# Kernel optimization log

Hardware: AMD Instinct MI355X
Metric: run time of the kernel (lower is better)

The kernel has to match this reference:

```python
import jax, jax.numpy as jnp
import numpy as np

B_, L_, D_ = 2, 1024, 2048
E_, N_, R_, K_ = 4096, 16, 128, 4
EPS = 1e-5


def setup_inputs() -> dict:
    key = jax.random.key(0)
    ks = jax.random.split(key, 12)
    s = lambda i, shape, scale=0.02: jax.random.normal(ks[i], shape, jnp.float32) * scale
    # dt bias init as in the module: inv_dt = dt + log(-expm1(-dt)), dt ~ logU[1e-3, 0.1]
    dt = jnp.exp(jax.random.uniform(ks[10], (E_,)) * (np.log(0.1) - np.log(0.001)) + np.log(0.001))
    inv_dt = dt + jnp.log(-jnp.expm1(-dt))
    return {
        'resid': jax.random.normal(ks[0], (B_, L_, D_), jnp.float32),
        'norm_w': jnp.ones((D_,), jnp.float32),
        'skip_w': s(1, (E_, D_)),
        'in_w': s(2, (E_, D_)),
        'conv_w': s(3, (E_, K_), 0.2),
        'conv_b': jnp.zeros((E_,), jnp.float32),
        'wd1': s(4, (R_, E_)),
        'wd2': s(5, (E_, R_), R_ ** -0.5),
        'wd2_b': inv_dt,
        'wB': s(6, (N_, E_)),
        'wC': s(7, (N_, E_)),
        'A_log': jnp.log(jnp.broadcast_to(jnp.arange(1, N_ + 1, dtype=jnp.float32), (E_, N_))),
        'W_D': jnp.ones((E_,), jnp.float32),
        'out_w': s(8, (D_, E_)),
    }


def _forward(resid, norm_w, skip_w, in_w, conv_w, conv_b, wd1, wd2, wd2_b,
             wB, wC, A_log, W_D, out_w):
    B, L, D = resid.shape
    E, K = conv_w.shape
    N = A_log.shape[1]
    # RMSNorm
    rn = resid * jax.lax.rsqrt(jnp.mean(resid * resid, -1, keepdims=True) + EPS) * norm_w
    skip = rn @ skip_w.T                       # [B,L,E] gate branch (z)
    x_in = rn @ in_w.T                         # [B,L,E]
    # depthwise causal conv1d (pad left K-1, truncate to L), then SiLU
    xp = jnp.pad(x_in, ((0, 0), (K - 1, 0), (0, 0)))
    conv = conv_b + sum(xp[:, k:k + L, :] * conv_w[:, k] for k in range(K))
    x = jax.nn.silu(conv)                      # [B,L,E] ssm input
    # low-rank delta, input-dependent B/C
    delta = jax.nn.softplus((x @ wd1.T) @ wd2.T + wd2_b)   # [B,L,E]
    A = -jnp.exp(A_log)                        # [E,N]
    Bm = x @ wB.T                              # [B,L,N]
    Cm = x @ wC.T                              # [B,L,N]

    def step(h, inp):
        d_l, b_l, c_l, x_l = inp               # [B,E],[B,N],[B,N],[B,E]
        h = jnp.exp(d_l[:, :, None] * A) * h + (d_l * x_l)[:, :, None] * b_l[:, None, :]
        y_l = jnp.einsum('ben,bn->be', h, c_l)
        return h, y_l

    h0 = jnp.zeros((B, E, N), resid.dtype)
    xs = (delta.transpose(1, 0, 2), Bm.transpose(1, 0, 2),
          Cm.transpose(1, 0, 2), x.transpose(1, 0, 2))
    _, ys = jax.lax.scan(step, h0, xs)         # ys: [L,B,E]
    y = ys.transpose(1, 0, 2) + x * W_D        # skip connection via D
    y = y * jax.nn.silu(skip)                  # gating
    return resid + y @ out_w.T                 # out_proj + residual


def reference(resid, norm_w, skip_w, in_w, conv_w, conv_b, wd1, wd2, wd2_b,
              wB, wC, A_log, W_D, out_w):
    return _forward(resid, norm_w, skip_w, in_w, conv_w, conv_b, wd1, wd2,
                    wd2_b, wB, wC, A_log, W_D, out_w)
```

## Files before the change

kernel.cpp:

```cpp
#include <hip/hip_runtime.h>
#include <stdint.h>

#define NB 2
#define NL 1024
#define ND 2048
#define NE 4096
#define NN 16
#define NR 128
#define NKC 4
#define NBL (NB*NL)
#define EPSV 1e-5f
#define SEG_T 256
#define SCAN_T 32

typedef __attribute__((ext_vector_type(4))) float f32x4;
typedef __attribute__((ext_vector_type(8))) short short8;
typedef __attribute__((ext_vector_type(8))) unsigned short ushort8;
typedef __attribute__((ext_vector_type(4))) unsigned short ushort4_t;
typedef __attribute__((ext_vector_type(2))) unsigned short ushort2_t;

__device__ __forceinline__ unsigned short f2bf(float f) {
  union { float f; unsigned u; } v; v.f = f;
  unsigned r = v.u + 0x7FFFu + ((v.u >> 16) & 1u);
  return (unsigned short)(r >> 16);
}

__device__ __forceinline__ float bf2f(unsigned short u) {
  union { unsigned u; float f; } v; v.u = (unsigned)u << 16; return v.f;
}

__device__ __forceinline__ void load_lds16(const void* g, void* l) {
  __builtin_amdgcn_global_load_lds((const __attribute__((address_space(1))) void*)g,
                                   (__attribute__((address_space(3))) void*)l,
                                   16, 0, 0);
}

__device__ __forceinline__ int swzmask(int row) {
  return ((row ^ (row >> 2)) & 3) * 8;
}

template<int CTRL>
__device__ __forceinline__ float dpp_mov(float v) {
  return __int_as_float(__builtin_amdgcn_update_dpp(
      0, __float_as_int(v), CTRL, 0xF, 0xF, true));
}

__global__ void rmsnorm_kernel(const float* __restrict__ resid,
                               const float* __restrict__ nw,
                               unsigned short* __restrict__ rn) {
  int row = blockIdx.x;
  int tid = threadIdx.x;
  const float* r = resid + (size_t)row * ND;
  f32x4 v0 = *(const f32x4*)(r + tid * 8);
  f32x4 v1 = *(const f32x4*)(r + tid * 8 + 4);
  float vals[8];
#pragma unroll
  for (int i = 0; i < 4; ++i) { vals[i] = v0[i]; vals[4 + i] = v1[i]; }
  float ss = 0.f;
#pragma unroll
  for (int i = 0; i < 8; ++i) ss += vals[i] * vals[i];
  for (int o = 32; o > 0; o >>= 1) ss += __shfl_down(ss, o);
  __shared__ float ps[4];
  if ((tid & 63) == 0) ps[tid >> 6] = ss;
  __syncthreads();
  float tot = ps[0] + ps[1] + ps[2] + ps[3];
  float scale = rsqrtf(tot / (float)ND + EPSV);
  ushort8 o8;
#pragma unroll
  for (int i = 0; i < 8; ++i) o8[i] = f2bf(vals[i] * scale * nw[tid * 8 + i]);
  *(ushort8*)(rn + (size_t)row * ND + tid * 8) = o8;
}

__global__ void cast_bf16_kernel(const float* __restrict__ in,
                                 unsigned short* __restrict__ out, int n8) {
  int i = blockIdx.x * blockDim.x + threadIdx.x;
  if (i >= n8) return;
  f32x4 a = *(const f32x4*)(in + (size_t)i * 8);
  f32x4 b = *(const f32x4*)(in + (size_t)i * 8 + 4);
  ushort8 o;
#pragma unroll
  for (int j = 0; j < 4; ++j) { o[j] = f2bf(a[j]); o[4 + j] = f2bf(b[j]); }
  *(ushort8*)(out + (size_t)i * 8) = o;
}

__global__ void build_wcat_kernel(const float* __restrict__ wd1,
                                  const float* __restrict__ wB,
                                  const float* __restrict__ wC,
                                  unsigned short* __restrict__ out) {
  int i = blockIdx.x * blockDim.x + threadIdx.x;
  if (i >= 256 * NE / 8) return;
  int col8 = i & (NE / 8 - 1);
  int row = i >> 9;
  const float* src = nullptr; int srow = 0;
  if (row < 128)      { src = wd1; srow = row; }
  else if (row < 144) { src = wB;  srow = row - 128; }
  else if (row < 160) { src = wC;  srow = row - 144; }
  ushort8 o;
  if (src) {
    f32x4 a = *(const f32x4*)(src + (size_t)srow * NE + col8 * 8);
    f32x4 b = *(const f32x4*)(src + (size_t)srow * NE + col8 * 8 + 4);
#pragma unroll
    for (int j = 0; j < 4; ++j) { o[j] = f2bf(a[j]); o[4 + j] = f2bf(b[j]); }
  } else {
#pragma unroll
    for (int j = 0; j < 8; ++j) o[j] = 0;
  }
  *(ushort8*)(out + (size_t)row * NE + col8 * 8) = o;
}

__global__ __launch_bounds__(512, 2)
void gemm256_fused(const unsigned short* __restrict__ A,
                   const unsigned short* __restrict__ B,
                   float* __restrict__ Gout,
                   unsigned short* __restrict__ Xout) {
  const int K = 2048, NH = K / 32;
  __shared__ unsigned short Asl[4][8192];
  __shared__ unsigned short Bsl[4][8192];
  int tid = threadIdx.x;
  int w = tid >> 6, lane = tid & 63;
  int wm = w >> 2, wn = w & 3;
  int lr = lane & 15, kg8 = (lane >> 4) * 8;
  int m0 = blockIdx.y * 256, n0 = blockIdx.x * 256;

  int srow = tid >> 2;
  int scol = ((tid & 3) * 8) ^ swzmask(srow);
  const unsigned short* ga = A + (size_t)(m0 + srow) * K + scol;
  const unsigned short* gb = B + (size_t)(n0 + srow) * K + scol;
  char* ldsA0 = (char*)&Asl[0][0] + w * 1024;
  char* ldsB0 = (char*)&Bsl[0][0] + w * 1024;

  auto stageA = [&](int h) {
    int slot = h & 3, k0 = h * 32;
    load_lds16(ga + k0, ldsA0 + slot * 16384);
    load_lds16(ga + k0 + (size_t)128 * K, ldsA0 + slot * 16384 + 8192);
  };
  auto stageB = [&](int h) {
    int slot = h & 3, k0 = h * 32;
    load_lds16(gb + k0, ldsB0 + slot * 16384);
    load_lds16(gb + k0 + (size_t)128 * K, ldsB0 + slot * 16384 + 8192);
  };

  f32x4 acc[8][4];
#pragma unroll
  for (int i = 0; i < 8; ++i)
#pragma unroll
    for (int j = 0; j < 4; ++j) acc[i][j] = (f32x4){0.f, 0.f, 0.f, 0.f};

  stageA(0); stageB(0); stageA(1); stageB(1); stageA(2); stageB(2);
  asm volatile("s_waitcnt vmcnt(8)" ::: "memory");
  __builtin_amdgcn_s_barrier();

  int fsw = swzmask(lr);
  int kgs = kg8 ^ fsw;

  for (int h = 0; h < NH; ++h) {
    int slot = h & 3;
    const unsigned short* As_ = &Asl[slot][0];
    const unsigned short* Bs_ = &Bsl[slot][0];
    int arow = wm * 128 + lr;
    int brow = wn * 64 + lr;
    short8 a[8], b[4];
#pragma unroll
    for (int i = 0; i < 4; ++i)
      a[i] = *(const short8*)&As_[(arow + i * 16) * 32 + kgs];
#pragma unroll
    for (int j = 0; j < 4; ++j)
      b[j] = *(const short8*)&Bs_[(brow + j * 16) * 32 + kgs];
    if (h + 3 < NH) stageA(h + 3);
    __builtin_amdgcn_s_barrier();
    __builtin_amdgcn_s_setprio(1);
#pragma unroll
    for (int i = 0; i < 4; ++i)
#pragma unroll
      for (int j = 0; j < 4; ++j)
        acc[i][j] = __builtin_amdgcn_mfma_f32_16x16x32_bf16(a[i], b[j], acc[i][j], 0, 0, 0);
    __builtin_amdgcn_s_setprio(0);
    __builtin_amdgcn_s_barrier();
#pragma unroll
    for (int i = 0; i < 4; ++i)
      a[4 + i] = *(const short8*)&As_[(arow + (4 + i) * 16) * 32 + kgs];
    if (h + 3 < NH) stageB(h + 3);
    __builtin_amdgcn_s_barrier();
    __builtin_amdgcn_s_setprio(1);
#pragma unroll
    for (int i = 0; i < 4; ++i)
#pragma unroll
      for (int j = 0; j < 4; ++j)
        acc[4 + i][j] = __builtin_amdgcn_mfma_f32_16x16x32_bf16(a[4 + i], b[j], acc[4 + i][j], 0, 0, 0);
    __builtin_amdgcn_s_setprio(0);
    if (h < NH - 3)       { asm volatile("s_waitcnt vmcnt(8)" ::: "memory"); }
    else if (h == NH - 3) { asm volatile("s_waitcnt vmcnt(4)" ::: "memory"); }
    else if (h == NH - 2) { asm volatile("s_waitcnt vmcnt(0)" ::: "memory"); }
    __builtin_amdgcn_s_barrier();
  }

  int rbase = m0 + wm * 128 + (lane >> 4) * 4;
  int cbase = n0 + wn * 64 + (lane & 15);
  bool isg = (n0 < 4096);
#pragma unroll
  for (int mf = 0; mf < 8; ++mf) {
#pragma unroll
    for (int nf = 0; nf < 4; ++nf) {
      int col = cbase + nf * 16;
#pragma unroll
      for (int rr = 0; rr < 4; ++rr) {
        int row = rbase + mf * 16 + rr;
        float v = acc[mf][nf][rr];
        if (isg) Gout[(size_t)row * 4096 + col] = v / (1.f + __expf(-v));
        else     Xout[(size_t)row * 4096 + (col - 4096)] = f2bf(v);
      }
    }
  }
}

template<int MODE>
__global__ __launch_bounds__(256)
void gemm_bt(const unsigned short* __restrict__ A,
             const unsigned short* __restrict__ B,
             float* __restrict__ C,
             int M, int N, int K, int ksteps_per_z,
             const float* __restrict__ bias) {
  __shared__ unsigned short As[3][128 * 32];
  __shared__ unsigned short Bs[3][128 * 32];
  int tid = threadIdx.x;
  int w = tid >> 6, lane = tid & 63;
  int m0 = blockIdx.y * 128, n0 = blockIdx.x * 128;
  int kz0 = blockIdx.z * ksteps_per_z * 32;
  if (MODE == 0) C += (size_t)blockIdx.z * M * N;
  const int NH = ksteps_per_z;

  f32x4 acc[4][4];
#pragma unroll
  for (int i = 0; i < 4; ++i)
#pragma unroll
    for (int j = 0; j < 4; ++j) acc[i][j] = (f32x4){0.f, 0.f, 0.f, 0.f};

  int wm = w >> 1, wn = w & 1;
  int lr = lane & 15, kg = lane >> 4;

  int fe0 = (w) * 512 + lane * 8;
  int fe1 = (4 + w) * 512 + lane * 8;
  int r0 = fe0 >> 5, c0 = fe0 & 31;
  int r1 = fe1 >> 5, c1 = fe1 & 31;
  int sc0 = c0 ^ swzmask(r0);
  int sc1 = c1 ^ swzmask(r1);
  const unsigned short* Ag0 = A + (size_t)(m0 + r0) * K + sc0 + kz0;
  const unsigned short* Ag1 = A + (size_t)(m0 + r1) * K + sc1 + kz0;
  const unsigned short* Bg0 = B + (size_t)(n0 + r0) * K + sc0 + kz0;
  const unsigned short* Bg1 = B + (size_t)(n0 + r1) * K + sc1 + kz0;

  auto stage = [&](int h) {
    int slot = h % 3, kk = h * 32;
    load_lds16(Ag0 + kk, &As[slot][(w) * 512]);
    load_lds16(Ag1 + kk, &As[slot][(4 + w) * 512]);
    load_lds16(Bg0 + kk, &Bs[slot][(w) * 512]);
    load_lds16(Bg1 + kk, &Bs[slot][(4 + w) * 512]);
  };

  stage(0);
  if (NH > 1) stage(1);

  int kgs = (kg * 8) ^ swzmask(lr);

  for (int h = 0; h < NH; ++h) {
    int slot = h % 3;
    __builtin_amdgcn_s_barrier();
    if (h + 2 < NH) stage(h + 2);
    int rem = NH - 1 - h;
    if (rem >= 2)      { asm volatile("s_waitcnt vmcnt(8)" ::: "memory"); }
    else if (rem == 1) { asm volatile("s_waitcnt vmcnt(4)" ::: "memory"); }
    else               { asm volatile("s_waitcnt vmcnt(0)" ::: "memory"); }
    __builtin_amdgcn_s_barrier();
    short8 a[4], b[4];
#pragma unroll
    for (int i = 0; i < 4; ++i)
      a[i] = *(const short8*)&As[slot][(wm * 64 + i * 16 + lr) * 32 + kgs];
#pragma unroll
    for (int j = 0; j < 4; ++j)
      b[j] = *(const short8*)&Bs[slot][(wn * 64 + j * 16 + lr) * 32 + kgs];
    __builtin_amdgcn_s_setprio(1);
#pragma unroll
    for (int i = 0; i < 4; ++i)
#pragma unroll
      for (int j = 0; j < 4; ++j)
        acc[i][j] = __builtin_amdgcn_mfma_f32_16x16x32_bf16(a[i], b[j], acc[i][j], 0, 0, 0);
    __builtin_amdgcn_s_setprio(0);
  }

#pragma unroll
  for (int i = 0; i < 4; ++i) {
#pragma unroll
    for (int j = 0; j < 4; ++j) {
      int rbase = m0 + wm * 64 + i * 16 + kg * 4;
      int col = n0 + wn * 64 + j * 16 + lr;
#pragma unroll
      for (int r = 0; r < 4; ++r) {
        float v = acc[i][j][r];
        size_t idx = (size_t)(rbase + r) * N + col;
        if (MODE == 0) {
          C[idx] = v;
        } else {
          float t = v + bias[col];
          ((unsigned short*)C)[idx] = f2bf((t > 20.f) ? t : log1pf(__expf(t)));
        }
      }
    }
  }
}

__global__ void reduce_out_kernel(const float* __restrict__ part,
                                  const float* __restrict__ resid,
                                  float* __restrict__ out) {
  size_t base = ((size_t)blockIdx.x * blockDim.x + threadIdx.x) * 4;
  if (base >= (size_t)NBL * ND) return;
  f32x4 r = *(const f32x4*)(resid + base);
#pragma unroll
  for (int z = 0; z < 4; ++z)
    r += *(const f32x4*)(part + (size_t)z * NBL * ND + base);
  *(f32x4*)(out + base) = r;
}

__global__ void conv_silu_kernel(const unsigned short* __restrict__ xin,
                                 const float* __restrict__ cw,
                                 const float* __restrict__ cb,
                                 unsigned short* __restrict__ xbf) {
  size_t idx = (size_t)blockIdx.x * blockDim.x + threadIdx.x;
  if (idx >= (size_t)NB * NL * NE) return;
  int e = (int)(idx & (NE - 1));
  int r = (int)(idx >> 12);
  int l = r & (NL - 1);
  float acc = cb[e];
#pragma unroll
  for (int k = 0; k < NKC; ++k) {
    int ls = l - 3 + k;
    if (ls >= 0) acc += bf2f(xin[(size_t)(r - 3 + k) * NE + e]) * cw[e * 4 + k];
  }
  float s = acc / (1.f + __expf(-acc));
  xbf[idx] = f2bf(s);
}

__global__ void reduce_tcat_kernel(const float* __restrict__ part,
                                   unsigned short* __restrict__ tbf,
                                   float* __restrict__ bc) {
  int idx = blockIdx.x * blockDim.x + threadIdx.x;
  if (idx >= NBL * 160) return;
  int m = idx / 160, c = idx - m * 160;
  float s = 0.f;
#pragma unroll
  for (int z = 0; z < 16; ++z) s += part[(size_t)z * NBL * 256 + (size_t)m * 256 + c];
  if (c < 128) tbf[m * 128 + c] = f2bf(s);
  else if (c < 144) bc[m * 32 + (c - 128)] = s;
  else bc[m * 32 + 16 + (c - 144)] = s;
}

__global__ __launch_bounds__(256)
void scan1_kernel(const unsigned short* __restrict__ delta_bf,
                  const unsigned short* __restrict__ x_bf,
                  const float* __restrict__ bc,
                  const float* __restrict__ gf,
                  const float* __restrict__ A_log,
                  const float* __restrict__ W_D,
                  unsigned short* __restrict__ yg,
                  float* __restrict__ fin,
                  float* __restrict__ dtot) {
  __shared__ unsigned short dxl[2][SCAN_T][2][16];
  __shared__ float gl[2][SCAN_T][16];
  __shared__ float BCl[2][SCAN_T][32];
  __shared__ float yl2[SCAN_T][16][2];
  __shared__ float wdl[16];
  int tid = threadIdx.x;
  int n = tid & 15, el = tid >> 4;
  int w = tid >> 6, lane = tid & 63;
  int e0 = blockIdx.x * 16;
  int b = blockIdx.y >> 2, seg = blockIdx.y & 3;
  int e = e0 + el;
  float A2 = -__expf(A_log[e * 16 + n]) * 1.44269504f;
  if (tid < 16) wdl[tid] = W_D[e0 + tid];
  float h = 0.f, cum = 0.f;

  const unsigned short* gdl = delta_bf + (size_t)b * NL * NE + e0;
  const unsigned short* gx  = x_bf + (size_t)b * NL * NE + e0;
  const float* gg  = gf + (size_t)b * NL * 4096 + e0;
  const float* gBC = bc + (size_t)b * NL * 32;

  const unsigned short* dxsrc = ((lane >> 1) & 1) ? gx : gdl;
  int dxrow = (w & 1) * 16 + (lane >> 2);
  int dxcol = (lane & 1) * 8;
  int grow = (w & 1) * 16 + (lane >> 2);
  int gcol = (lane & 3) * 4;
  int bcrow = w * 8 + (lane >> 3);
  int bccol = (lane & 7) * 4;
  int nloads = (seg == 0 || w < 2) ? 2 : 1;

  auto stage = [&](int buf, int c) {
    int l0 = seg * SEG_T + c * SCAN_T;
    if (w < 2)
      load_lds16(dxsrc + (size_t)(l0 + dxrow) * NE + dxcol, &dxl[buf][(w & 1) * 16][0][0]);
    else if (seg == 0)
      load_lds16(gg + (size_t)(l0 + grow) * 4096 + gcol, &gl[buf][(w & 1) * 16][0]);
    load_lds16(gBC + (size_t)(l0 + bcrow) * 32 + bccol, &BCl[buf][w * 8][0]);
  };

  stage(0, 0);
  const int nch = SEG_T / SCAN_T;
  for (int c = 0; c < nch; ++c) {
    int cur = c & 1;
    if (c + 1 < nch) {
      stage(cur ^ 1, c + 1);
      if (nloads == 2) { asm volatile("s_waitcnt vmcnt(2)" ::: "memory"); }
      else             { asm volatile("s_waitcnt vmcnt(1)" ::: "memory"); }
    } else {
      asm volatile("s_waitcnt vmcnt(0)" ::: "memory");
    }
    __syncthreads();
    const unsigned short (*dxc)[2][16] = dxl[cur];
    const float (*BCc)[32] = BCl[cur];
#pragma unroll 8
    for (int t = 0; t < SCAN_T; ++t) {
      float dc = bf2f(dxc[t][0][el]);
      float xc = bf2f(dxc[t][1][el]);
      float Bc = BCc[t][n];
      float Cc = BCc[t][16 + n];
      cum += dc;
      float a = dc * A2, ed;
      asm("v_exp_f32 %0, %1" : "=v"(ed) : "v"(a));
      h = ed * h + (dc * xc) * Bc;
      float p = h * Cc;
      p += dpp_mov<0xB1>(p);
      p += dpp_mov<0x4E>(p);
      p += dpp_mov<0x141>(p);
      if ((n & 7) == 0) yl2[t][el][n >> 3] = p;
    }
    __syncthreads();
    {
      int t = tid >> 3, part = tid & 7;
      int l0 = seg * SEG_T + c * SCAN_T;
      ushort2_t o;
#pragma unroll
      for (int j = 0; j < 2; ++j) {
        int ee = part * 2 + j;
        float xv = bf2f(dxc[t][1][ee]);
        float y = yl2[t][ee][0] + yl2[t][ee][1] + xv * wdl[ee];
        if (seg == 0) y *= gl[cur][t][ee];
        o[j] = f2bf(y);
      }
      *(ushort2_t*)(yg + (size_t)(b * NL + l0 + t) * NE + e0 + part * 2) = o;
    }
    __syncthreads();
  }
  fin[(size_t)((seg * 2 + b) * 4096 + e) * 16 + n] = h;
  if (n == 0) dtot[(size_t)(seg * 2 + b) * 4096 + e] = cum;
}

__global__ __launch_bounds__(256)
void scan2_kernel(const unsigned short* __restrict__ delta_bf,
                  unsigned short* __restrict__ yg,
                  const float* __restrict__ bc,
                  const float* __restrict__ gf,
                  const float* __restrict__ A_log,
                  const float* __restrict__ fin,
                  const float* __restrict__ dtot) {
  __shared__ unsigned short dl[2][SCAN_T][16];
  __shared__ unsigned short ypl[2][SCAN_T][16];
  __shared__ float Cl[2][SCAN_T][16];
  __shared__ float gl2[2][SCAN_T][16];
  __shared__ float ycl[SCAN_T][16][2];
  int tid = threadIdx.x;
  int n = tid & 15, el = tid >> 4;
  int w = tid >> 6, lane = tid & 63;
  int e0 = blockIdx.x * 16;
  int b = blockIdx.y / 3, seg = 1 + blockIdx.y % 3;
  int e = e0 + el;
  float A2 = -__expf(A_log[e * 16 + n]) * 1.44269504f;
  float h = fin[(size_t)(b * 4096 + e) * 16 + n];
  for (int s2 = 1; s2 < seg; ++s2) {
    float dt = dtot[(size_t)(s2 * 2 + b) * 4096 + e];
    float a = A2 * dt, pw;
    asm("v_exp_f32 %0, %1" : "=v"(pw) : "v"(a));
    h = fin[(size_t)((s2 * 2 + b) * 4096 + e) * 16 + n] + pw * h;
  }

  const unsigned short* gd = delta_bf + (size_t)b * NL * NE + e0;
  unsigned short* gy = yg + (size_t)b * NL * NE + e0;
  const float* gg  = gf + (size_t)b * NL * 4096 + e0;
  const float* gBC = bc + (size_t)b * NL * 32;

  int dyrow = lane >> 1;
  int dycol = (lane & 1) * 8;
  int crow = (w & 1) * 16 + (lane >> 2);
  int ccol = 16 + (lane & 3) * 4;
  int grow = (w & 1) * 16 + (lane >> 2);
  int gcol = (lane & 3) * 4;
  int nloads = (w < 2) ? 2 : 1;

  auto stage = [&](int buf, int c) {
    int l0 = seg * SEG_T + c * SCAN_T;
    if (w == 0)      load_lds16(gd + (size_t)(l0 + dyrow) * NE + dycol, &dl[buf][0][0]);
    else if (w == 1) load_lds16(gy + (size_t)(l0 + dyrow) * NE + dycol, &ypl[buf][0][0]);
    if (w < 2) load_lds16(gBC + (size_t)(l0 + crow) * 32 + ccol, &Cl[buf][(w & 1) * 16][0]);
    else       load_lds16(gg + (size_t)(l0 + grow) * 4096 + gcol, &gl2[buf][(w & 1) * 16][0]);
  };

  stage(0, 0);
  float cum = 0.f;
  const int nch = SEG_T / SCAN_T;
  for (int c = 0; c < nch; ++c) {
    int cur = c & 1;
    if (c + 1 < nch) {
      stage(cur ^ 1, c + 1);
      if (nloads == 2) { asm volatile("s_waitcnt vmcnt(2)" ::: "memory"); }
      else             { asm volatile("s_waitcnt vmcnt(1)" ::: "memory"); }
    } else {
      asm volatile("s_waitcnt vmcnt(0)" ::: "memory");
    }
    __syncthreads();
    const unsigned short (*dc_)[16] = dl[cur];
    const float (*Cc_)[16] = Cl[cur];
#pragma unroll 8
    for (int t = 0; t < SCAN_T; ++t) {
      float dcv = bf2f(dc_[t][el]);
      cum += dcv;
      float a = A2 * cum, pw;
      asm("v_exp_f32 %0, %1" : "=v"(pw) : "v"(a));
      float p = (pw * h) * Cc_[t][n];
      p += dpp_mov<0xB1>(p);
      p += dpp_mov<0x4E>(p);
      p += dpp_mov<0x141>(p);
      if ((n & 7) == 0) ycl[t][el][n >> 3] = p;
    }
    __syncthreads();
    {
      int t = tid >> 3, part = tid & 7;
      int l0 = seg * SEG_T + c * SCAN_T;
      ushort2_t o;
#pragma unroll
      for (int j = 0; j < 2; ++j) {
        int ee = part * 2 + j;
        float y = ycl[t][ee][0] + ycl[t][ee][1] + bf2f(ypl[cur][t][ee]);
        o[j] = f2bf(y * gl2[cur][t][ee]);
      }
      *(ushort2_t*)(gy + (size_t)(l0 + t) * NE + part * 2) = o;
    }
    __syncthreads();
  }
}

extern "C" void kernel_launch(void* const* d_in, const int* in_sizes, int n_in,
                              void* d_out, int out_size, void* d_ws, size_t ws_size,
                              hipStream_t stream) {
  const float* resid  = (const float*)d_in[0];
  const float* norm_w = (const float*)d_in[1];
  const float* skip_w = (const float*)d_in[2];
  const float* in_w   = (const float*)d_in[3];
  const float* conv_w = (const float*)d_in[4];
  const float* conv_b = (const float*)d_in[5];
  const float* wd1    = (const float*)d_in[6];
  const float* wd2    = (const float*)d_in[7];
  const float* wd2_b  = (const float*)d_in[8];
  const float* wB     = (const float*)d_in[9];
  const float* wC     = (const float*)d_in[10];
  const float* A_log  = (const float*)d_in[11];
  const float* W_D    = (const float*)d_in[12];
  const float* out_w  = (const float*)d_in[13];
  float* out = (float*)d_out;

  char* ws = (char*)d_ws;
  size_t off = 0;
  auto alloc = [&](size_t bytes) -> void* {
    void* p = ws + off;
    off += (bytes + 255) & ~(size_t)255;
    return p;
  };
  unsigned short* rn_bf      = (unsigned short*)alloc((size_t)NBL * ND * 2);
  unsigned short* wskipin_bf = (unsigned short*)alloc((size_t)2 * NE * ND * 2);
  unsigned short* wout_bf    = (unsigned short*)alloc((size_t)ND * NE * 2);
  unsigned short* wd2_bf     = (unsigned short*)alloc((size_t)NE * NR * 2);
  unsigned short* wcat_bf    = (unsigned short*)alloc((size_t)256 * NE * 2);
  float* g_f                 = (float*)alloc((size_t)NBL * NE * 4);
  unsigned short* xin_bf     = (unsigned short*)alloc((size_t)NBL * NE * 2);
  unsigned short* x_bf       = (unsigned short*)alloc((size_t)NBL * NE * 2);
  float* part_f              = (float*)alloc((size_t)16 * NBL * 256 * 4);
  unsigned short* t_bf       = (unsigned short*)alloc((size_t)NBL * NR * 2);
  float* bc_f                = (float*)alloc((size_t)NBL * 32 * 4);
  unsigned short* yg_bf      = (unsigned short*)alloc((size_t)NBL * NE * 2);
  float* fin_f               = (float*)alloc((size_t)4 * NB * NE * 16 * 4);
  float* dtot_f              = (float*)alloc((size_t)4 * NB * NE * 4);
  unsigned short* delta_bf = wskipin_bf;
  float* part2_f = g_f;
  (void)ws_size; (void)in_sizes; (void)n_in; (void)out_size;

  rmsnorm_kernel<<<dim3(NBL), dim3(256), 0, stream>>>(resid, norm_w, rn_bf);

  cast_bf16_kernel<<<dim3((NE * ND / 8 + 255) / 256), dim3(256), 0, stream>>>(skip_w, wskipin_bf, NE * ND / 8);
  cast_bf16_kernel<<<dim3((NE * ND / 8 + 255) / 256), dim3(256), 0, stream>>>(in_w, wskipin_bf + (size_t)NE * ND, NE * ND / 8);
  cast_bf16_kernel<<<dim3((ND * NE / 8 + 255) / 256), dim3(256), 0, stream>>>(out_w, wout_bf, ND * NE / 8);
  cast_bf16_kernel<<<dim3((NE * NR / 8 + 255) / 256), dim3(256), 0, stream>>>(wd2, wd2_bf, NE * NR / 8);
  build_wcat_kernel<<<dim3(256 * NE / 8 / 256), dim3(256), 0, stream>>>(wd1, wB, wC, wcat_bf);

  gemm256_fused<<<dim3(8192 / 256, NBL / 256), dim3(512), 0, stream>>>(
      rn_bf, wskipin_bf, g_f, xin_bf);

  conv_silu_kernel<<<dim3((int)(((size_t)NB * NL * NE) / 256)), dim3(256), 0, stream>>>(
      xin_bf, conv_w, conv_b, x_bf);

  gemm_bt<0><<<dim3(256 / 128, NBL / 128, 16), dim3(256), 0, stream>>>(
      x_bf, wcat_bf, part_f, NBL, 256, NE, (NE / 32) / 16, nullptr);
  reduce_tcat_kernel<<<dim3((NBL * 160 + 255) / 256), dim3(256), 0, stream>>>(
      part_f, t_bf, bc_f);

  gemm_bt<1><<<dim3(NE / 128, NBL / 128, 1), dim3(256), 0, stream>>>(
      t_bf, wd2_bf, (float*)delta_bf, NBL, NE, NR, NR / 32, wd2_b);

  scan1_kernel<<<dim3(NE / 16, NB * 4), dim3(256), 0, stream>>>(
      delta_bf, x_bf, bc_f, g_f, A_log, W_D, yg_bf, fin_f, dtot_f);
  scan2_kernel<<<dim3(NE / 16, NB * 3), dim3(256), 0, stream>>>(
      delta_bf, yg_bf, bc_f, g_f, A_log, fin_f, dtot_f);

  gemm_bt<0><<<dim3(ND / 128, NBL / 128, 4), dim3(256), 0, stream>>>(
      yg_bf, wout_bf, part2_f, NBL, ND, NE, (NE / 32) / 4, nullptr);
  reduce_out_kernel<<<dim3((int)((size_t)NBL * ND / 4 / 256)), dim3(256), 0, stream>>>(
      part2_f, resid, out);
}
```

Baseline: 412.8 us.

## Restructure fused GEMM pipeline to triple-buffered, single-barrier quarter-step schedule

Replaces the 4-slot LDS ring with 3 slots and a prefetch depth of two k-steps. Each k-step now needs only one barrier, and the global-to-LDS loads are split into four quarter stages interleaved with four MFMA sub-blocks that reorder the B fragment loads. The swizzled LDS addressing is dropped in favour of plain row-major offsets. This is meant to reduce barrier overhead and LDS footprint, which may allow more occupancy. In exchange it risks LDS bank conflicts without the swizzle and less prefetch latency hiding.

```diff
diff --git a/kernel.cpp b/kernel.cpp
--- a/kernel.cpp
+++ b/kernel.cpp
@@ -114,31 +114,27 @@
                    float* __restrict__ Gout,
                    unsigned short* __restrict__ Xout) {
   const int K = 2048, NH = K / 32;
-  __shared__ unsigned short Asl[4][8192];
-  __shared__ unsigned short Bsl[4][8192];
+  __shared__ unsigned short Asl[3][256 * 32];
+  __shared__ unsigned short Bsl[3][256 * 32];
   int tid = threadIdx.x;
   int w = tid >> 6, lane = tid & 63;
   int wm = w >> 2, wn = w & 3;
   int lr = lane & 15, kg8 = (lane >> 4) * 8;
   int m0 = blockIdx.y * 256, n0 = blockIdx.x * 256;
 
-  int srow = tid >> 2;
-  int scol = ((tid & 3) * 8) ^ swzmask(srow);
+  int srow = tid >> 2, scol = (tid & 3) * 8;
   const unsigned short* ga = A + (size_t)(m0 + srow) * K + scol;
   const unsigned short* gb = B + (size_t)(n0 + srow) * K + scol;
-  char* ldsA0 = (char*)&Asl[0][0] + w * 1024;
-  char* ldsB0 = (char*)&Bsl[0][0] + w * 1024;
-
-  auto stageA = [&](int h) {
-    int slot = h & 3, k0 = h * 32;
-    load_lds16(ga + k0, ldsA0 + slot * 16384);
-    load_lds16(ga + k0 + (size_t)128 * K, ldsA0 + slot * 16384 + 8192);
+
+  auto stageHalf = [&](int bufS, int t, int j) {
+    int k0 = t * 32;
+    if (j < 2)
+      load_lds16(ga + (size_t)j * 128 * K + k0,
+                 (char*)&Asl[bufS][0] + j * 8192 + w * 1024);
+    else
+      load_lds16(gb + (size_t)(j - 2) * 128 * K + k0,
+                 (char*)&Bsl[bufS][0] + (j - 2) * 8192 + w * 1024);
   };
-  auto stageB = [&](int h) {
-    int slot = h & 3, k0 = h * 32;
-    load_lds16(gb + k0, ldsB0 + slot * 16384);
-    load_lds16(gb + k0 + (size_t)128 * K, ldsB0 + slot * 16384 + 8192);
-  };
 
   f32x4 acc[8][4];
 #pragma unroll
@@ -146,52 +142,69 @@
 #pragma unroll
     for (int j = 0; j < 4; ++j) acc[i][j] = (f32x4){0.f, 0.f, 0.f, 0.f};
 
-  stageA(0); stageB(0); stageA(1); stageB(1); stageA(2); stageB(2);
-  asm volatile("s_waitcnt vmcnt(8)" ::: "memory");
-  __builtin_amdgcn_s_barrier();
-
-  int fsw = swzmask(lr);
-  int kgs = kg8 ^ fsw;
-
-  for (int h = 0; h < NH; ++h) {
-    int slot = h & 3;
-    const unsigned short* As_ = &Asl[slot][0];
-    const unsigned short* Bs_ = &Bsl[slot][0];
-    int arow = wm * 128 + lr;
-    int brow = wn * 64 + lr;
+#pragma unroll
+  for (int j = 0; j < 4; ++j) stageHalf(0, 0, j);
+#pragma unroll
+  for (int j = 0; j < 4; ++j) stageHalf(1, 1, j);
+
+  int buf = 0, bufS = 2;
+  int arow = wm * 128 + lr;
+  int brow = wn * 64 + lr;
+
+  for (int t = 0; t < NH; ++t) {
+    if (t + 1 < NH) { asm volatile("s_waitcnt vmcnt(4)" ::: "memory"); }
+    else            { asm volatile("s_waitcnt vmcnt(0)" ::: "memory"); }
+    __builtin_amdgcn_s_barrier();
+    const unsigned short* As_ = &Asl[buf][0];
+    const unsigned short* Bs_ = &Bsl[buf][0];
+    bool st = (t + 2 < NH);
     short8 a[8], b[4];
 #pragma unroll
     for (int i = 0; i < 4; ++i)
-      a[i] = *(const short8*)&As_[(arow + i * 16) * 32 + kgs];
-#pragma unroll
-    for (int j = 0; j < 4; ++j)
-      b[j] = *(const short8*)&Bs_[(brow + j * 16) * 32 + kgs];
-    if (h + 3 < NH) stageA(h + 3);
-    __builtin_amdgcn_s_barrier();
+      a[i] = *(const short8*)&As_[(arow + i * 16) * 32 + kg8];
+#pragma unroll
+    for (int j = 0; j < 2; ++j)
+      b[j] = *(const short8*)&Bs_[(brow + j * 16) * 32 + kg8];
+    if (st) stageHalf(bufS, t + 2, 0);
     __builtin_amdgcn_s_setprio(1);
 #pragma unroll
     for (int i = 0; i < 4; ++i)
 #pragma unroll
-      for (int j = 0; j < 4; ++j)
+      for (int j = 0; j < 2; ++j)
         acc[i][j] = __builtin_amdgcn_mfma_f32_16x16x32_bf16(a[i], b[j], acc[i][j], 0, 0, 0);
     __builtin_amdgcn_s_setprio(0);
-    __builtin_amdgcn_s_barrier();
+#pragma unroll
+    for (int j = 2; j < 4; ++j)
+      b[j] = *(const short8*)&Bs_[(brow + j * 16) * 32 + kg8];
+    if (st) stageHalf(bufS, t + 2, 1);
+    __builtin_amdgcn_s_setprio(1);
 #pragma unroll
     for (int i = 0; i < 4; ++i)
-      a[4 + i] = *(const short8*)&As_[(arow + (4 + i) * 16) * 32 + kgs];
-    if (h + 3 < NH) stageB(h + 3);
-    __builtin_amdgcn_s_barrier();
+#pragma unroll
+      for (int j = 2; j < 4; ++j)
+        acc[i][j] = __builtin_amdgcn_mfma_f32_16x16x32_bf16(a[i], b[j], acc[i][j], 0, 0, 0);
+    __builtin_amdgcn_s_setprio(0);
+#pragma unroll
+    for (int i = 4; i < 8; ++i)
+      a[i] = *(const short8*)&As_[(arow + i * 16) * 32 + kg8];
+    if (st) stageHalf(bufS, t + 2, 2);
     __builtin_amdgcn_s_setprio(1);
 #pragma unroll
-    for (int i = 0; i < 4; ++i)
-#pragma unroll
-      for (int j = 0; j < 4; ++j)
-        acc[4 + i][j] = __builtin_amdgcn_mfma_f32_16x16x32_bf16(a[4 + i], b[j], acc[4 + i][j], 0, 0, 0);
+    for (int i = 4; i < 8; ++i)
+#pragma unroll
+      for (int j = 2; j < 4; ++j)
+        acc[i][j] = __builtin_amdgcn_mfma_f32_16x16x32_bf16(a[i], b[j], acc[i][j], 0, 0, 0);
     __builtin_amdgcn_s_setprio(0);
-    if (h < NH - 3)       { asm volatile("s_waitcnt vmcnt(8)" ::: "memory"); }
-    else if (h == NH - 3) { asm volatile("s_waitcnt vmcnt(4)" ::: "memory"); }
-    else if (h == NH - 2) { asm volatile("s_waitcnt vmcnt(0)" ::: "memory"); }
-    __builtin_amdgcn_s_barrier();
+    if (st) stageHalf(bufS, t + 2, 3);
+    __builtin_amdgcn_s_setprio(1);
+#pragma unroll
+    for (int i = 4; i < 8; ++i)
+#pragma unroll
+      for (int j = 0; j < 2; ++j)
+        acc[i][j] = __builtin_amdgcn_mfma_f32_16x16x32_bf16(a[i], b[j], acc[i][j], 0, 0, 0);
+    __builtin_amdgcn_s_setprio(0);
+    buf  = (buf  == 2) ? 0 : buf  + 1;
+    bufS = (bufS == 2) ? 0 : bufS + 1;
   }
 
   int rbase = m0 + wm * 128 + (lane >> 4) * 4;
```

After: 411.9 us. About the same (-0.2%).
